# Performance work log

Hardware: AMD Instinct MI355X
Metric: run time of the kernel (lower is better)

The kernel has to match this reference:

```python
import jax, jax.numpy as jnp
import numpy as np
from jax import lax

B, D, H, W = 4, 32, 256, 256
ALPHA = 4.0     # init arg alpha
KFRAMES = 4.0   # self.K = alpha
EPS_BN = 1e-5

def FT2d(a):
    return jnp.fft.fft2(a, axes=(-2, -1))

def iFT2d(a):
    return jnp.fft.ifft2(a, axes=(-2, -1))

def forward_proj(field, otf):
    # field [B,D,H,W] real, otf [B,D,H,W] complex -> min-max scaled |holo| [B,1,H,W]
    Fholo = jnp.sum(FT2d(field.astype(jnp.complex64)) * otf, axis=1, keepdims=True)
    holo = jnp.abs(iFT2d(Fholo))
    mn = holo.min(axis=(-2, -1), keepdims=True)
    mx = holo.max(axis=(-2, -1), keepdims=True)
    return (holo - mn) / (mx - mn)

def back_proj(holo, otf):
    # holo [B,1,H,W] real -> real field [B,D,H,W]; broadcasting over depth == tile+FFT
    Fh = FT2d(holo.astype(jnp.complex64))
    return jnp.real(iFT2d(Fh * jnp.conj(otf)))

def cbl(xin, w, g, b, act):
    y = lax.conv_general_dilated(xin, w, (1, 1), 'SAME',
                                 dimension_numbers=('NCHW', 'OIHW', 'NCHW'))
    m = y.mean(axis=(0, 2, 3), keepdims=True)
    v = y.var(axis=(0, 2, 3), keepdims=True)  # biased var, torch BN training-mode
    y = (y - m) * lax.rsqrt(v + EPS_BN) * g[None, :, None, None] + b[None, :, None, None]
    return jax.nn.leaky_relu(y, 0.01) if act else y

def resblock(xin, wa, ga, ba, wb, gb, bb):
    h = cbl(cbl(xin, wa, ga, ba, True), wb, gb, bb, False)
    return jax.nn.leaky_relu(xin + h, 0.01)

def plholonet_forward(phi, z, u1, u2, otf, K1f, rho1, rho2, soft_thr, p):
    # ---- X update: FFT-domain proximal solve ----
    x1 = phi - u1
    x2 = z - u2
    n = rho1 * back_proj(x1, otf) + rho2 * x2
    d = (rho2 + jnp.abs(otf) ** 2 * rho1).astype(jnp.complex64)
    x = jnp.real(iFT2d(FT2d(n.astype(jnp.complex64)) / d))
    # ---- Phi update: vectorized 30-step masked bisection ----
    phi_tilde = forward_proj(x, otf) + u1
    K0 = 1.0 - K1f
    c = ALPHA / KFRAMES
    def func(y):
        return c * (K0 - K1f / (jnp.exp(c * y) - 1.0)) + rho1 * (y - phi_tilde)
    ind0_init = K1f == 0
    phimin = jnp.full_like(phi_tilde, 1e-5)
    phimax = jnp.full_like(phi_tilde, 100.0)
    phiave = 0.5 * (phimin + phimax)
    def step(carry, _):
        pmin, pmax, pave, ind0 = carry
        ind1 = jnp.logical_not(ind0)
        t = func(pave)
        pmin = jnp.where((t > 0) & ind1, pave, pmin)
        pmax = jnp.where((t < 0) & ind1, pave, pmax)
        ind0 = ind0 | ((t == 0) & ind1)
        pave = jnp.where(jnp.logical_not(ind0), 0.5 * (pmin + pmax), pave)
        return (pmin, pmax, pave, ind0), None
    (_, _, phiave, _), _ = lax.scan(step, (phimin, phimax, phiave, ind0_init), None, length=30)
    phi_next = jnp.where(ind0_init, phi_tilde - K0 / rho1, phiave)
    # ---- Z update: denoiser with symmetry loss ----
    z_tilde = x + u2
    h1 = resblock(z_tilde, p['w1a'], p['g1a'], p['b1a'], p['w1b'], p['g1b'], p['b1b'])
    h1_thr = jnp.sign(h1) * jax.nn.relu(jnp.abs(h1) - soft_thr)
    z_next = resblock(h1_thr, p['w2a'], p['g2a'], p['b2a'], p['w2b'], p['g2b'], p['b2b'])
    x_fb = resblock(h1, p['w2a'], p['g2a'], p['b2a'], p['w2b'], p['g2b'], p['b2b'])
    stage_symloss = x_fb - z_tilde
    # ---- dual updates ----
    u1_next = u1 + phi_next - forward_proj(x, otf)
    u2_next = u2 + z_next - x
    return (x, phi_next, z_next, u1_next, u2_next, stage_symloss)

def setup_inputs() -> dict:
    key = jax.random.key(0)
    ks = jax.random.split(key, 16)
    f = jnp.float32
    inp = dict(
        x=jax.random.normal(ks[0], (B, D, H, W), f),
        phi=jax.random.uniform(ks[1], (B, 1, H, W), dtype=f),
        z=jax.random.normal(ks[2], (B, D, H, W), f) * 0.1,
        u1=jax.random.uniform(ks[3], (B, 1, H, W), dtype=f) * 0.1,
        u2=jax.random.uniform(ks[4], (B, D, H, W), dtype=f) * 0.1,
        otf_real=jax.random.normal(ks[5], (B, D, H, W), f) * 0.5,
        otf_imag=jax.random.normal(ks[6], (B, D, H, W), f) * 0.5,
        K1=jax.random.randint(ks[7], (B, 1, H, W), 0, 5, jnp.int32),
        rho1=jnp.array([0.7], f),
        rho2=jnp.array([0.5], f),
        soft_thr=jnp.array([0.01], f),
    )
    for i, sfx in enumerate(['1a', '1b', '2a', '2b']):
        inp['w' + sfx] = jax.random.normal(ks[8 + i], (D, D, 3, 3), f) * 0.05
        inp['g' + sfx] = jnp.ones((D,), f)
        inp['b' + sfx] = jnp.zeros((D,), f)
    return inp

def reference(x, phi, z, u1, u2, otf_real, otf_imag, K1, rho1, rho2, soft_thr,
              w1a, g1a, b1a, w1b, g1b, b1b, w2a, g2a, b2a, w2b, g2b, b2b):
    # note: the torch forward immediately overwrites its `x` argument via X_update,
    # so the input x is unused (kept in the signature for interface faithfulness).
    otf = (otf_real + 1j * otf_imag).astype(jnp.complex64)
    K1f = K1.astype(jnp.float32)
    p = dict(w1a=w1a, g1a=g1a, b1a=b1a, w1b=w1b, g1b=g1b, b1b=b1b,
             w2a=w2a, g2a=g2a, b2a=b2a, w2b=w2b, g2b=g2b, b2b=b2b)
    return plholonet_forward(phi, z, u1, u2, otf, K1f, rho1, rho2, soft_thr, p)
```

## Files before the change

kernel.cpp:

```cpp
#include <hip/hip_runtime.h>
#include <math.h>

#define WDIM 256
#define HW   65536

struct cplx { float x, y; };
__device__ __forceinline__ cplx cmul(cplx a, cplx b){ return {a.x*b.x - a.y*b.y, a.x*b.y + a.y*b.x}; }
__device__ __forceinline__ cplx cadd(cplx a, cplx b){ return {a.x+b.x, a.y+b.y}; }
__device__ __forceinline__ cplx csub(cplx a, cplx b){ return {a.x-b.x, a.y-b.y}; }
__device__ __forceinline__ void swapc(cplx& a, cplx& b){ cplx t=a; a=b; b=t; }

typedef __attribute__((ext_vector_type(8))) short short8;
typedef __attribute__((ext_vector_type(4))) float float4v;

__device__ __forceinline__ unsigned short f2bf(float f){
  unsigned int u = __float_as_uint(f);
  unsigned int r = (u + 0x7FFFu + ((u >> 16) & 1u)) >> 16;
  return (unsigned short)r;
}
__device__ __forceinline__ float bf2f(unsigned short h){
  return __uint_as_float(((unsigned int)h) << 16);
}

template<bool INV>
__device__ __forceinline__ void fft16(cplx v[16]) {
  const float C16[8] = {1.f, 0.9238795325112867f, 0.7071067811865476f, 0.3826834323650898f,
                        0.f, -0.3826834323650898f, -0.7071067811865476f, -0.9238795325112867f};
  const float S16[8] = {0.f, 0.3826834323650898f, 0.7071067811865476f, 0.9238795325112867f,
                        1.f, 0.9238795325112867f, 0.7071067811865476f, 0.3826834323650898f};
  swapc(v[1], v[8]); swapc(v[2], v[4]); swapc(v[3], v[12]);
  swapc(v[5], v[10]); swapc(v[7], v[14]); swapc(v[11], v[13]);
  #pragma unroll
  for (int s = 1; s <= 4; ++s) {
    const int m = 1 << s, half = m >> 1, step = 16 >> s;
    #pragma unroll
    for (int k = 0; k < 16; k += m) {
      #pragma unroll
      for (int j = 0; j < half; ++j) {
        cplx w = {C16[j*step], INV ? S16[j*step] : -S16[j*step]};
        cplx t = cmul(w, v[k+j+half]);
        v[k+j+half] = csub(v[k+j], t);
        v[k+j]      = cadd(v[k+j], t);
      }
    }
  }
}

template<bool INV>
__device__ void fft256_16(cplx v[16], int t, cplx* Yu) {
  fft16<INV>(v);
  float ang = (INV ? 6.283185307179586f : -6.283185307179586f) * (float)t * (1.0f/256.0f);
  float sn, cs; sincosf(ang, &sn, &cs);
  cplx wstep = {cs, sn}, w = {1.f, 0.f};
  #pragma unroll
  for (int c = 0; c < 16; ++c) { v[c] = cmul(v[c], w); w = cmul(w, wstep); }
  __syncthreads();
  #pragma unroll
  for (int c = 0; c < 16; ++c) Yu[t*17 + c] = v[c];
  __syncthreads();
  cplx z[16];
  #pragma unroll
  for (int b = 0; b < 16; ++b) z[b] = Yu[b*17 + t];
  fft16<INV>(z);
  #pragma unroll
  for (int d = 0; d < 16; ++d) v[d] = z[d];
  __syncthreads();
}

__global__ __launch_bounds__(256) void k_row_fwd_all(const float* __restrict__ a,
                                                     const float* __restrict__ b,
                                                     const float* __restrict__ sa,
                                                     const float* __restrict__ sb,
                                                     cplx* __restrict__ P,
                                                     cplx* __restrict__ XS,
                                                     const float* __restrict__ w1a,
                                                     const float* __restrict__ w1b,
                                                     const float* __restrict__ w2a,
                                                     const float* __restrict__ w2b,
                                                     unsigned short* __restrict__ Ap) {
  __shared__ cplx Y[16*280];
  int bp = blockIdx.y;
  if (bp == 66) {
    int base = blockIdx.x * 2304;
    for (int r = threadIdx.x; r < 2304; r += 256) {
      int idx = base + r;
      int wsel = idx / 9216, rr = idx - wsel*9216;
      const float* w = wsel==0 ? w1a : wsel==1 ? w1b : wsel==2 ? w2a : w2b;
      int tap = rr / 1024, r2 = rr - tap*1024, oc = r2 >> 5, ic = r2 & 31;
      Ap[idx] = f2bf(w[(oc*32 + ic)*9 + tap]);
    }
    return;
  }
  int unit = threadIdx.x >> 4, t = threadIdx.x & 15;
  size_t rowoff = (size_t)(blockIdx.x*16 + unit)*WDIM;
  const float *pa, *pb;
  size_t base0, baseo_rel;
  cplx* outb;
  if (bp < 64) {
    int bb = bp >> 4, p = bp & 15;
    pa = a; pb = b;
    base0 = ((size_t)(bb*32 + 2*p))*HW + rowoff;
    outb = P; baseo_rel = (size_t)bp*HW + rowoff;
  } else {
    int pp = bp - 64;
    pa = sa; pb = sb;
    base0 = ((size_t)(2*pp))*HW + rowoff;
    outb = XS; baseo_rel = (size_t)pp*HW + rowoff;
  }
  size_t base1 = base0 + HW;
  cplx v[16];
  #pragma unroll
  for (int i = 0; i < 16; ++i) {
    size_t o = i*16 + t;
    v[i] = {pa[base0+o] - pb[base0+o], pa[base1+o] - pb[base1+o]};
  }
  fft256_16<false>(v, t, Y + unit*280);
  #pragma unroll
  for (int d = 0; d < 16; ++d) outb[baseo_rel + t + 16*d] = v[d];
}

template<bool INV>
__device__ void col_core(const cplx* __restrict__ in, cplx* lds, cplx v[16], size_t planeBase) {
  int tid = threadIdx.x;
  #pragma unroll
  for (int i = 0; i < 16; ++i) {
    int idx = tid + 256*i; int h = idx >> 4, w = idx & 15;
    lds[h*17 + w] = in[planeBase + (size_t)h*WDIM + w];
  }
  __syncthreads();
  int u = tid >> 4, t = tid & 15;
  cplx vv[16];
  #pragma unroll
  for (int a = 0; a < 16; ++a) vv[a] = lds[(16*a + t)*17 + u];
  fft256_16<INV>(vv, t, lds + u*280);
  #pragma unroll
  for (int d = 0; d < 16; ++d) v[d] = vv[d];
}

__global__ __launch_bounds__(256) void k_col_fwd_all(cplx* __restrict__ P,
                                                     cplx* __restrict__ XS) {
  __shared__ cplx lds[4480];
  int y = blockIdx.y;
  cplx* buf = (y < 64) ? (P + (size_t)y*HW) : (XS + (size_t)(y-64)*HW);
  size_t planeBase = blockIdx.x*16;
  cplx v[16];
  col_core<false>(buf, lds, v, planeBase);
  int u = threadIdx.x >> 4, t = threadIdx.x & 15;
  #pragma unroll
  for (int d = 0; d < 16; ++d) lds[(t + 16*d)*17 + u] = v[d];
  __syncthreads();
  int tid = threadIdx.x;
  #pragma unroll
  for (int i = 0; i < 16; ++i) {
    int idx = tid + 256*i; int h = idx >> 4, w = idx & 15;
    buf[planeBase + (size_t)h*WDIM + w] = lds[h*17 + w];
  }
}

__global__ __launch_bounds__(256) void k_combine_inv(const cplx* __restrict__ P,
                                                     const cplx* __restrict__ XS,
                                                     const float* __restrict__ otr,
                                                     const float* __restrict__ oti,
                                                     const float* __restrict__ r1p,
                                                     const float* __restrict__ r2p,
                                                     cplx* __restrict__ W2,
                                                     cplx* __restrict__ HFX) {
  __shared__ cplx R[16*273];
  int kw = threadIdx.x;
  int kh = blockIdx.x;
  int b  = blockIdx.y;
  int kh2 = (256 - kh) & 255;
  int kw2 = (256 - kw) & 255;
  int k  = (kh << 8) | kw;
  int k2 = (kh2 << 8) | kw2;
  float rho1 = r1p[0], rho2 = r2p[0];
  int c = b >> 1, par = b & 1;
  cplx Sk = XS[(c << 16) | k], Sm = XS[(c << 16) | k2];
  cplx A;
  if (par == 0) A = {0.5f*(Sk.x + Sm.x), 0.5f*(Sk.y - Sm.y)};
  else          A = {0.5f*(Sk.y + Sm.y), 0.5f*(Sm.x - Sk.x)};
  cplx Am = {A.x, -A.y};
  float hfr = 0.f, hfi = 0.f, hfr2 = 0.f, hfi2 = 0.f;
  int unit = threadIdx.x >> 4, t = threadIdx.x & 15;

  #pragma unroll 1
  for (int half = 0; half < 2; ++half) {
    #pragma unroll 1
    for (int pl = 0; pl < 8; ++pl) {
      int p = half*8 + pl;
      int pb = (b*16 + p) << 16;
      cplx Pk = P[pb | k], Pm = P[pb | k2];
      float Zr[2], Zi[2];
      Zr[0] = 0.5f*(Pk.x + Pm.x); Zi[0] = 0.5f*(Pk.y - Pm.y);
      Zr[1] = 0.5f*(Pk.y + Pm.y); Zi[1] = 0.5f*(Pm.x - Pk.x);
      float Xr[2], Xi[2];
      #pragma unroll
      for (int dd = 0; dd < 2; ++dd) {
        int db = (b*32 + 2*p + dd) << 16;
        float or1 = otr[db | k],  oi1 = oti[db | k];
        float or2 = otr[db | k2], oi2 = oti[db | k2];
        float Gr = 0.5f*(A.x*or1 + A.y*oi1 + Am.x*or2 + Am.y*oi2);
        float Gi = 0.5f*(A.y*or1 - A.x*oi1 + Am.x*oi2 - Am.y*or2);
        float di = 0.5f*(1.f/(rho2 + rho1*(or1*or1 + oi1*oi1))
                       + 1.f/(rho2 + rho1*(or2*or2 + oi2*oi2)));
        float xr = (rho1*Gr + rho2*Zr[dd])*di;
        float xi = (rho1*Gi + rho2*Zi[dd])*di;
        Xr[dd] = xr; Xi[dd] = xi;
        hfr  += xr*or1 - xi*oi1;
        hfi  += xr*oi1 + xi*or1;
        hfr2 += xr*or2 + xi*oi2;
        hfi2 += xr*oi2 - xi*or2;
      }
      R[(pl*2)*273 + kw]    = {Xr[0] - Xi[1], Xi[0] + Xr[1]};
      R[(pl*2+1)*273 + kw2] = {Xr[0] + Xi[1], Xr[1] - Xi[0]};
    }
    __syncthreads();
    {
      cplx* slot = R + unit*273;
      cplx v[16];
      #pragma unroll
      for (int i = 0; i < 16; ++i) v[i] = slot[i*16 + t];
      fft256_16<true>(v, t, slot);
      int plane = b*16 + half*8 + (unit >> 1);
      int row = (unit & 1) ? kh2 : kh;
      size_t base = (size_t)plane*HW + (size_t)row*WDIM;
      #pragma unroll
      for (int d = 0; d < 16; ++d)
        W2[base + t + 16*d] = {v[d].x*(1.f/256.f), v[d].y*(1.f/256.f)};
    }
  }
  R[0*273 + kw]  = {hfr,  hfi};
  R[1*273 + kw2] = {hfr2, hfi2};
  __syncthreads();
  {
    cplx* slot = R + (unit & 1)*273;
    cplx v[16];
    #pragma unroll
    for (int i = 0; i < 16; ++i) v[i] = slot[i*16 + t];
    fft256_16<true>(v, t, slot);
    if (unit < 2) {
      int row = unit ? kh2 : kh;
      size_t base = (size_t)b*HW + (size_t)row*WDIM;
      #pragma unroll
      for (int d = 0; d < 16; ++d)
        HFX[base + t + 16*d] = {v[d].x*(1.f/256.f), v[d].y*(1.f/256.f)};
    }
  }
}

__global__ __launch_bounds__(256) void k_col_inv_all(const cplx* __restrict__ W2,
                                                     const cplx* __restrict__ XS,
                                                     const float* __restrict__ u2,
                                                     float* __restrict__ xout,
                                                     unsigned short* __restrict__ ztcl,
                                                     float* __restrict__ holo,
                                                     float* __restrict__ partials) {
  __shared__ cplx lds[4480];
  int y = blockIdx.y;
  int tid = threadIdx.x;
  if (y < 64) {
    int bb = y >> 4, p = y & 15;
    cplx v[16];
    col_core<true>(W2 + (size_t)y*HW, lds, v, blockIdx.x*16);
    int u = tid >> 4, t = tid & 15;
    #pragma unroll
    for (int d = 0; d < 16; ++d) lds[(t + 16*d)*17 + u] = {v[d].x*(1.f/256.f), v[d].y*(1.f/256.f)};
    __syncthreads();
    size_t out0 = ((size_t)(bb*32 + 2*p))*HW + blockIdx.x*16;
    size_t out1 = out0 + HW;
    #pragma unroll
    for (int i = 0; i < 16; ++i) {
      int idx = tid + 256*i; int h = idx >> 4, w = idx & 15;
      cplx val = lds[h*17 + w];
      size_t g0 = out0 + (size_t)h*WDIM + w;
      size_t g1 = out1 + (size_t)h*WDIM + w;
      float zt0 = val.x + u2[g0];
      float zt1 = val.y + u2[g1];
      xout[g0] = val.x;
      xout[g1] = val.y;
      int pix = (h << 8) + (blockIdx.x << 4) + w;
      unsigned int pk = ((unsigned int)f2bf(zt1) << 16) | (unsigned int)f2bf(zt0);
      *(unsigned int*)(ztcl + ((((size_t)(bb << 16)) + pix) << 5) + 2*p) = pk;
    }
  } else {
    int py = y - 64;
    float* ldsf = (float*)lds;
    cplx v[16];
    col_core<true>(XS + (size_t)py*HW, lds, v, blockIdx.x*16);
    int u = tid >> 4, t = tid & 15;
    #pragma unroll
    for (int d = 0; d < 16; ++d) {
      float re = v[d].x*(1.f/256.f), im = v[d].y*(1.f/256.f);
      ldsf[(t + 16*d)*17 + u] = sqrtf(re*re + im*im);
    }
    __syncthreads();
    float mn = 1e30f, mx = -1e30f;
    size_t planeBase = (size_t)py*HW + blockIdx.x*16;
    #pragma unroll
    for (int i = 0; i < 16; ++i) {
      int idx = tid + 256*i; int h = idx >> 4, w = idx & 15;
      float val = ldsf[h*17 + w];
      holo[planeBase + (size_t)h*WDIM + w] = val;
      mn = fminf(mn, val); mx = fmaxf(mx, val);
    }
    __syncthreads();
    #pragma unroll
    for (int s = 1; s < 64; s <<= 1) { mn = fminf(mn, __shfl_xor(mn, s)); mx = fmaxf(mx, __shfl_xor(mx, s)); }
    if ((tid & 63) == 0) { ldsf[(tid>>6)*2] = mn; ldsf[(tid>>6)*2 + 1] = mx; }
    __syncthreads();
    if (tid == 0) {
      float a = fminf(fminf(ldsf[0], ldsf[2]), fminf(ldsf[4], ldsf[6]));
      float b = fmaxf(fmaxf(ldsf[1], ldsf[3]), fmaxf(ldsf[5], ldsf[7]));
      partials[(py*16 + blockIdx.x)*2]     = a;
      partials[(py*16 + blockIdx.x)*2 + 1] = b;
    }
  }
}

__global__ __launch_bounds__(256) void k_bisect(const float* __restrict__ holo,
                                                const float* __restrict__ partials,
                                                const float* __restrict__ u1,
                                                const int* __restrict__ K1,
                                                const float* __restrict__ r1p,
                                                float* __restrict__ phi_out,
                                                float* __restrict__ u1_out) {
  __shared__ float red2[2];
  int i = blockIdx.x*256 + threadIdx.x;
  int b = i >> 16;
  if (threadIdx.x < 16) {
    float mn = partials[(b*16 + threadIdx.x)*2];
    float mx = partials[(b*16 + threadIdx.x)*2 + 1];
    #pragma unroll
    for (int s = 1; s < 16; s <<= 1) { mn = fminf(mn, __shfl_xor(mn, s)); mx = fmaxf(mx, __shfl_xor(mx, s)); }
    if (threadIdx.x == 0) { red2[0] = mn; red2[1] = mx; }
  }
  __syncthreads();
  float mn = red2[0], mx = red2[1];
  float fp = (holo[i] - mn) / (mx - mn);
  float pt = fp + u1[i];
  float K1f = (float)K1[i];
  float K0 = 1.f - K1f;
  float rho1 = r1p[0];
  bool ind0i = (K1f == 0.f);
  bool ind0 = ind0i;
  float pmin = 1e-5f, pmax = 100.f, pave = 0.5f*(pmin + pmax);
  #pragma unroll 1
  for (int it = 0; it < 30; ++it) {
    float e = expf(pave);
    float t = (K0 - K1f/(e - 1.f)) + rho1*(pave - pt);
    bool ind1 = !ind0;
    if (t > 0.f && ind1) pmin = pave;
    if (t < 0.f && ind1) pmax = pave;
    ind0 = ind0 || (t == 0.f && ind1);
    if (!ind0) pave = 0.5f*(pmin + pmax);
  }
  float pn = ind0i ? (pt - K0/rho1) : pave;
  phi_out[i] = pn;
  u1_out[i]  = u1[i] + pn - fp;
}

#define CONV_R 4
__global__ __launch_bounds__(256, 4) void k_conv(const unsigned short* __restrict__ inCL,
                                                 const unsigned short* __restrict__ Aprep,
                                                 unsigned short* __restrict__ outCL,
                                                 float* __restrict__ part,
                                                 int mode,
                                                 const float* __restrict__ scsh,
                                                 const float* __restrict__ thrp) {
  __shared__ unsigned short tile[6*66*32];
  __shared__ float sred[4][16][2];
  int tid = threadIdx.x;
  int bx = blockIdx.x, by = blockIdx.y, bz = blockIdx.z;
  int w0 = bx*64, h0 = by*CONV_R;

  for (int idx = tid; idx < 6*264; idx += 256) {
    int lrow = idx/264, rem = idx - lrow*264;
    int lcol = rem >> 2, m = rem & 3;
    int grow = h0 - 1 + lrow, gcol = w0 - 1 + lcol;
    uint4 val = {0,0,0,0};
    if (grow >= 0 && grow < 256 && gcol >= 0 && gcol < 256) {
      uint4 raw = *(const uint4*)(inCL + (((size_t)(bz<<16) + (grow<<8) + gcol)<<5) + m*8);
      if (mode == 0) val = raw;
      else {
        unsigned short h8[8]; *(uint4*)h8 = raw;
        #pragma unroll
        for (int j = 0; j < 8; ++j) {
          float v = bf2f(h8[j]);
          int ic = m*8+j; v = v*scsh[ic] + scsh[32+ic]; v = v > 0.f ? v : 0.01f*v;
          h8[j] = f2bf(v);
        }
        val = *(uint4*)h8;
      }
    }
    *(uint4*)&tile[(size_t)idx*8] = val;
  }

  int lane = tid & 63, w = tid >> 6;
  int q = lane >> 4, ln = lane & 15;
  int ocH = w & 1, s0 = w >> 1;
  short8 afrag[9];
  #pragma unroll
  for (int t = 0; t < 9; ++t)
    afrag[t] = *(const short8*)(Aprep + ((t*32 + ocH*16 + ln)*32 + q*8));
  __syncthreads();

  float sacc[4] = {0,0,0,0}, s2acc[4] = {0,0,0,0};
  #pragma unroll
  for (int r = 0; r < CONV_R; ++r) {
    #pragma unroll
    for (int si = 0; si < 2; ++si) {
      int s = s0 + si*2;
      float4v acc = {0.f, 0.f, 0.f, 0.f};
      #pragma unroll
      for (int t = 0; t < 9; ++t) {
        int dy = t/3, dx = t - dy*3;
        int lrow = r + dy, lcol = s*16 + ln + dx;
        const short8 bfrag = *(const short8*)&tile[(lrow*66 + lcol)*32 + q*8];
        acc = __builtin_amdgcn_mfma_f32_16x16x32_bf16(afrag[t], bfrag, acc, 0, 0, 0);
      }
      int px = w0 + s*16 + ln, row = h0 + r;
      size_t obase = ((((size_t)(bz<<16) + (row<<8) + px))<<5) + ocH*16 + q*4;
      unsigned short o4[4];
      #pragma unroll
      for (int u = 0; u < 4; ++u) { o4[u] = f2bf(acc[u]); sacc[u] += acc[u]; s2acc[u] += acc[u]*acc[u]; }
      *(uint2*)(outCL + obase) = *(uint2*)o4;
    }
  }

  #pragma unroll
  for (int u = 0; u < 4; ++u) {
    float a = sacc[u], b2 = s2acc[u];
    #pragma unroll
    for (int mq = 1; mq < 16; mq <<= 1) { a += __shfl_xor(a, mq); b2 += __shfl_xor(b2, mq); }
    if (ln == 0) { sred[w][q*4+u][0] = a; sred[w][q*4+u][1] = b2; }
  }
  __syncthreads();
  if (tid < 64) {
    int ocH2 = tid >> 5, i16 = (tid >> 1) & 15, st = tid & 1;
    float tot = sred[ocH2][i16][st] + sred[ocH2+2][i16][st];
    int oc = ocH2*16 + i16;
    int blk = ((bz<<6) + by)*4 + bx;
    part[(oc*2+st)*1024 + blk] = tot;
  }
}

__global__ __launch_bounds__(256, 3) void k_conv35(const unsigned short* __restrict__ ztcl,
                                                   const unsigned short* __restrict__ c2,
                                                   const unsigned short* __restrict__ Aprep,
                                                   unsigned short* __restrict__ outT,
                                                   unsigned short* __restrict__ outR,
                                                   float* __restrict__ partT,
                                                   float* __restrict__ partR,
                                                   const float* __restrict__ ss1,
                                                   const float* __restrict__ thrp) {
  __shared__ unsigned short tileR[6*66*32];
  __shared__ unsigned short tileT[6*66*32];
  __shared__ float sredT[4][16][2];
  __shared__ float sredR[4][16][2];
  int tid = threadIdx.x;
  int bx = blockIdx.x, by = blockIdx.y, bz = blockIdx.z;
  int w0 = bx*64, h0 = by*CONV_R;
  float thr = thrp[0];

  for (int idx = tid; idx < 6*264; idx += 256) {
    int lrow = idx/264, rem = idx - lrow*264;
    int lcol = rem >> 2, m = rem & 3;
    int grow = h0 - 1 + lrow, gcol = w0 - 1 + lcol;
    uint4 rawv = {0,0,0,0}, thrv = {0,0,0,0};
    if (grow >= 0 && grow < 256 && gcol >= 0 && gcol < 256) {
      size_t gaddr = (((size_t)(bz<<16) + (grow<<8) + gcol)<<5) + m*8;
      uint4 az = *(const uint4*)(ztcl + gaddr);
      uint4 ac = *(const uint4*)(c2 + gaddr);
      unsigned short z8[8], cc8[8], h8[8], t8[8];
      *(uint4*)z8 = az; *(uint4*)cc8 = ac;
      #pragma unroll
      for (int j = 0; j < 8; ++j) {
        int ic = m*8 + j;
        float v = bf2f(z8[j]) + bf2f(cc8[j])*ss1[ic] + ss1[32+ic];
        v = v > 0.f ? v : 0.01f*v;
        h8[j] = f2bf(v);
        float hb = bf2f(h8[j]);
        float s = fabsf(hb) - thr; s = s > 0.f ? s : 0.f;
        t8[j] = f2bf(copysignf(s, hb));
      }
      rawv = *(uint4*)h8;
      thrv = *(uint4*)t8;
    }
    *(uint4*)&tileR[(size_t)idx*8] = rawv;
    *(uint4*)&tileT[(size_t)idx*8] = thrv;
  }

  int lane = tid & 63, w = tid >> 6;
  int q = lane >> 4, ln = lane & 15;
  int ocH = w & 1, s0 = w >> 1;
  short8 afrag[9];
  #pragma unroll
  for (int t = 0; t < 9; ++t)
    afrag[t] = *(const short8*)(Aprep + ((t*32 + ocH*16 + ln)*32 + q*8));
  __syncthreads();

  float saT[4] = {0,0,0,0}, s2T[4] = {0,0,0,0};
  float saR[4] = {0,0,0,0}, s2R[4] = {0,0,0,0};
  #pragma unroll
  for (int r = 0; r < CONV_R; ++r) {
    #pragma unroll
    for (int si = 0; si < 2; ++si) {
      int s = s0 + si*2;
      float4v accT = {0.f,0.f,0.f,0.f}, accR = {0.f,0.f,0.f,0.f};
      #pragma unroll
      for (int t = 0; t < 9; ++t) {
        int dy = t/3, dx = t - dy*3;
        int lrow = r + dy, lcol = s*16 + ln + dx;
        size_t off = ((size_t)(lrow*66 + lcol))*32 + q*8;
        const short8 bT = *(const short8*)&tileT[off];
        accT = __builtin_amdgcn_mfma_f32_16x16x32_bf16(afrag[t], bT, accT, 0, 0, 0);
        const short8 bR = *(const short8*)&tileR[off];
        accR = __builtin_amdgcn_mfma_f32_16x16x32_bf16(afrag[t], bR, accR, 0, 0, 0);
      }
      int px = w0 + s*16 + ln, row = h0 + r;
      size_t obase = ((((size_t)(bz<<16) + (row<<8) + px))<<5) + ocH*16 + q*4;
      unsigned short oT[4], oR[4];
      #pragma unroll
      for (int u = 0; u < 4; ++u) {
        oT[u] = f2bf(accT[u]); saT[u] += accT[u]; s2T[u] += accT[u]*accT[u];
        oR[u] = f2bf(accR[u]); saR[u] += accR[u]; s2R[u] += accR[u]*accR[u];
      }
      *(uint2*)(outT + obase) = *(uint2*)oT;
      *(uint2*)(outR + obase) = *(uint2*)oR;
    }
  }

  #pragma unroll
  for (int u = 0; u < 4; ++u) {
    float aT = saT[u], bT2 = s2T[u], aR = saR[u], bR2 = s2R[u];
    #pragma unroll
    for (int mq = 1; mq < 16; mq <<= 1) {
      aT += __shfl_xor(aT, mq); bT2 += __shfl_xor(bT2, mq);
      aR += __shfl_xor(aR, mq); bR2 += __shfl_xor(bR2, mq);
    }
    if (ln == 0) {
      sredT[w][q*4+u][0] = aT; sredT[w][q*4+u][1] = bT2;
      sredR[w][q*4+u][0] = aR; sredR[w][q*4+u][1] = bR2;
    }
  }
  __syncthreads();
  if (tid < 64) {
    int ocH2 = tid >> 5, i16 = (tid >> 1) & 15, st = tid & 1;
    int oc = ocH2*16 + i16;
    int blk = ((bz<<6) + by)*4 + bx;
    partT[(oc*2+st)*1024 + blk] = sredT[ocH2][i16][st] + sredT[ocH2+2][i16][st];
    partR[(oc*2+st)*1024 + blk] = sredR[ocH2][i16][st] + sredR[ocH2+2][i16][st];
  }
}

__global__ __launch_bounds__(256, 4) void k_conv_pair(const unsigned short* __restrict__ inA,
                                                      const unsigned short* __restrict__ inB,
                                                      unsigned short* __restrict__ outA,
                                                      unsigned short* __restrict__ outB,
                                                      float* __restrict__ partA,
                                                      float* __restrict__ partB,
                                                      const float* __restrict__ ssA,
                                                      const float* __restrict__ ssB,
                                                      const unsigned short* __restrict__ Aprep) {
  __shared__ unsigned short tile[6*66*32];
  __shared__ float sred[4][16][2];
  int tid = threadIdx.x;
  int bx = blockIdx.x, by = blockIdx.y;
  int half = blockIdx.z >> 2, bz = blockIdx.z & 3;
  const unsigned short* inCL = half ? inB : inA;
  unsigned short* outCL = half ? outB : outA;
  const float* scsh = half ? ssB : ssA;
  float* part = half ? partB : partA;
  int w0 = bx*64, h0 = by*CONV_R;

  for (int idx = tid; idx < 6*264; idx += 256) {
    int lrow = idx/264, rem = idx - lrow*264;
    int lcol = rem >> 2, m = rem & 3;
    int grow = h0 - 1 + lrow, gcol = w0 - 1 + lcol;
    uint4 val = {0,0,0,0};
    if (grow >= 0 && grow < 256 && gcol >= 0 && gcol < 256) {
      uint4 raw = *(const uint4*)(inCL + (((size_t)(bz<<16) + (grow<<8) + gcol)<<5) + m*8);
      unsigned short h8[8]; *(uint4*)h8 = raw;
      #pragma unroll
      for (int j = 0; j < 8; ++j) {
        float v = bf2f(h8[j]);
        int ic = m*8+j; v = v*scsh[ic] + scsh[32+ic]; v = v > 0.f ? v : 0.01f*v;
        h8[j] = f2bf(v);
      }
      val = *(uint4*)h8;
    }
    *(uint4*)&tile[(size_t)idx*8] = val;
  }

  int lane = tid & 63, w = tid >> 6;
  int q = lane >> 4, ln = lane & 15;
  int ocH = w & 1, s0 = w >> 1;
  short8 afrag[9];
  #pragma unroll
  for (int t = 0; t < 9; ++t)
    afrag[t] = *(const short8*)(Aprep + ((t*32 + ocH*16 + ln)*32 + q*8));
  __syncthreads();

  float sacc[4] = {0,0,0,0}, s2acc[4] = {0,0,0,0};
  #pragma unroll
  for (int r = 0; r < CONV_R; ++r) {
    #pragma unroll
    for (int si = 0; si < 2; ++si) {
      int s = s0 + si*2;
      float4v acc = {0.f, 0.f, 0.f, 0.f};
      #pragma unroll
      for (int t = 0; t < 9; ++t) {
        int dy = t/3, dx = t - dy*3;
        int lrow = r + dy, lcol = s*16 + ln + dx;
        const short8 bfrag = *(const short8*)&tile[(lrow*66 + lcol)*32 + q*8];
        acc = __builtin_amdgcn_mfma_f32_16x16x32_bf16(afrag[t], bfrag, acc, 0, 0, 0);
      }
      int px = w0 + s*16 + ln, row = h0 + r;
      size_t obase = ((((size_t)(bz<<16) + (row<<8) + px))<<5) + ocH*16 + q*4;
      unsigned short o4[4];
      #pragma unroll
      for (int u = 0; u < 4; ++u) { o4[u] = f2bf(acc[u]); sacc[u] += acc[u]; s2acc[u] += acc[u]*acc[u]; }
      *(uint2*)(outCL + obase) = *(uint2*)o4;
    }
  }

  #pragma unroll
  for (int u = 0; u < 4; ++u) {
    float a = sacc[u], b2 = s2acc[u];
    #pragma unroll
    for (int mq = 1; mq < 16; mq <<= 1) { a += __shfl_xor(a, mq); b2 += __shfl_xor(b2, mq); }
    if (ln == 0) { sred[w][q*4+u][0] = a; sred[w][q*4+u][1] = b2; }
  }
  __syncthreads();
  if (tid < 64) {
    int ocH2 = tid >> 5, i16 = (tid >> 1) & 15, st = tid & 1;
    float tot = sred[ocH2][i16][st] + sred[ocH2+2][i16][st];
    int oc = ocH2*16 + i16;
    int blk = ((bz<<6) + by)*4 + bx;
    part[(oc*2+st)*1024 + blk] = tot;
  }
}

__global__ __launch_bounds__(256) void k_finstats2(const float* __restrict__ part,
                                                   const float* __restrict__ g,
                                                   const float* __restrict__ beta,
                                                   float* __restrict__ SS) {
  __shared__ float red[8];
  int oc = blockIdx.x, t = threadIdx.x;
  const float* ps = part + oc*2048;
  float s  = ps[t] + ps[t+256] + ps[t+512] + ps[t+768];
  float s2 = ps[1024+t] + ps[1280+t] + ps[1536+t] + ps[1792+t];
  #pragma unroll
  for (int m = 1; m < 64; m <<= 1) { s += __shfl_xor(s, m); s2 += __shfl_xor(s2, m); }
  if ((t & 63) == 0) { red[(t>>6)*2] = s; red[(t>>6)*2+1] = s2; }
  __syncthreads();
  if (t == 0) {
    float S  = red[0] + red[2] + red[4] + red[6];
    float S2 = red[1] + red[3] + red[5] + red[7];
    const float N = 262144.f;
    float mean = S / N;
    float var  = S2 / N - mean*mean;
    float sc = g[oc] * rsqrtf(var + 1e-5f);
    SS[oc] = sc; SS[32+oc] = beta[oc] - mean*sc;
  }
}

__global__ __launch_bounds__(256) void k_finstats_dual(const float* __restrict__ pA,
                                                       const float* __restrict__ pB,
                                                       const float* __restrict__ g,
                                                       const float* __restrict__ beta,
                                                       float* __restrict__ SSa,
                                                       float* __restrict__ SSc) {
  __shared__ float red[8];
  int bxi = blockIdx.x;
  const float* part = bxi < 32 ? pA : pB;
  float* SS = bxi < 32 ? SSa : SSc;
  int oc = bxi & 31, t = threadIdx.x;
  const float* ps = part + oc*2048;
  float s  = ps[t] + ps[t+256] + ps[t+512] + ps[t+768];
  float s2 = ps[1024+t] + ps[1280+t] + ps[1536+t] + ps[1792+t];
  #pragma unroll
  for (int m = 1; m < 64; m <<= 1) { s += __shfl_xor(s, m); s2 += __shfl_xor(s2, m); }
  if ((t & 63) == 0) { red[(t>>6)*2] = s; red[(t>>6)*2+1] = s2; }
  __syncthreads();
  if (t == 0) {
    float S  = red[0] + red[2] + red[4] + red[6];
    float S2 = red[1] + red[3] + red[5] + red[7];
    const float N = 262144.f;
    float mean = S / N;
    float var  = S2 / N - mean*mean;
    float sc = g[oc] * rsqrtf(var + 1e-5f);
    SS[oc] = sc; SS[32+oc] = beta[oc] - mean*sc;
  }
}

__global__ __launch_bounds__(256) void k_finalAB(const unsigned short* __restrict__ ztcl,
                                                 const unsigned short* __restrict__ c2,
                                                 const unsigned short* __restrict__ c4,
                                                 const unsigned short* __restrict__ c6,
                                                 const float* __restrict__ SS1,
                                                 const float* __restrict__ SS4,
                                                 const float* __restrict__ SS6,
                                                 const float* __restrict__ thrp,
                                                 const float* __restrict__ x,
                                                 float* __restrict__ zout,
                                                 float* __restrict__ u2out,
                                                 float* __restrict__ symout) {
  __shared__ float zT[32*66];
  __shared__ float uT[32*66];
  __shared__ float sT[32*66];
  int tid = threadIdx.x;
  size_t b = blockIdx.y;
  int px0 = blockIdx.x*64;
  float thr = thrp[0];
  int px = tid >> 2, cg = tid & 3;
  size_t cbase = ((((b<<16) + px0 + px))<<5) + cg*8;
  uint4 za  = *(const uint4*)(ztcl + cbase);
  uint4 c2a = *(const uint4*)(c2 + cbase);
  uint4 c4a = *(const uint4*)(c4 + cbase);
  uint4 c6a = *(const uint4*)(c6 + cbase);
  unsigned short zs[8], c2s[8], c4s[8], c6s[8];
  *(uint4*)zs = za; *(uint4*)c2s = c2a; *(uint4*)c4s = c4a; *(uint4*)c6s = c6a;
  #pragma unroll
  for (int j = 0; j < 8; ++j) {
    int c = cg*8+j;
    float ztv = bf2f(zs[j]);
    float h0 = ztv + bf2f(c2s[j])*SS1[c] + SS1[32+c];
    h0 = h0 > 0.f ? h0 : 0.01f*h0;
    float hv = bf2f(f2bf(h0));
    float s = fabsf(hv) - thr; s = s > 0.f ? s : 0.f;
    float th = copysignf(s, hv);
    float zv = th + bf2f(c4s[j])*SS4[c] + SS4[32+c];
    zv = zv > 0.f ? zv : 0.01f*zv;
    float xv = hv + bf2f(c6s[j])*SS6[c] + SS6[32+c];
    xv = xv > 0.f ? xv : 0.01f*xv;
    zT[c*66 + px] = zv;
    uT[c*66 + px] = zv + ztv;
    sT[c*66 + px] = xv - ztv;
  }
  __syncthreads();
  #pragma unroll
  for (int i = 0; i < 2; ++i) {
    int ch = tid + i*256; int c = ch >> 4, p4 = (ch & 15)*4;
    size_t g = ((b*32 + c)<<16) + px0 + p4;
    float4 xv = *(const float4*)(x + g);
    float4 zv = { zT[c*66+p4], zT[c*66+p4+1], zT[c*66+p4+2], zT[c*66+p4+3] };
    float4 un = { uT[c*66+p4]   - 2.f*xv.x, uT[c*66+p4+1] - 2.f*xv.y,
                  uT[c*66+p4+2] - 2.f*xv.z, uT[c*66+p4+3] - 2.f*xv.w };
    float4 sv = { sT[c*66+p4], sT[c*66+p4+1], sT[c*66+p4+2], sT[c*66+p4+3] };
    *(float4*)(zout + g) = zv;
    *(float4*)(u2out + g) = un;
    *(float4*)(symout + g) = sv;
  }
}

extern "C" void kernel_launch(void* const* d_in, const int* in_sizes, int n_in,
                              void* d_out, int out_size, void* d_ws, size_t ws_size,
                              hipStream_t stream) {
  const float* phi  = (const float*)d_in[1];
  const float* z    = (const float*)d_in[2];
  const float* u1   = (const float*)d_in[3];
  const float* u2   = (const float*)d_in[4];
  const float* otr  = (const float*)d_in[5];
  const float* oti  = (const float*)d_in[6];
  const int*   K1   = (const int*)d_in[7];
  const float* rho1 = (const float*)d_in[8];
  const float* rho2 = (const float*)d_in[9];
  const float* sthr = (const float*)d_in[10];
  const float* w1a = (const float*)d_in[11];
  const float* g1a = (const float*)d_in[12];
  const float* b1a = (const float*)d_in[13];
  const float* w1b = (const float*)d_in[14];
  const float* g1b = (const float*)d_in[15];
  const float* b1b = (const float*)d_in[16];
  const float* w2a = (const float*)d_in[17];
  const float* g2a = (const float*)d_in[18];
  const float* b2a = (const float*)d_in[19];
  const float* w2b = (const float*)d_in[20];
  const float* g2b = (const float*)d_in[21];
  const float* b2b = (const float*)d_in[22];

  float* out = (float*)d_out;
  float* x_out   = out;
  float* phi_out = out + 8388608;
  float* z_out   = out + 8650752;
  float* u1_out  = out + 17039360;
  float* u2_out  = out + 17301504;
  float* sym_out = out + 25690112;

  char* ws = (char*)d_ws;
  cplx*  P     = (cplx*)ws;
  cplx*  XS    = (cplx*)(ws + 67108864);
  cplx*  HFX   = (cplx*)(ws + 69206016);
  float* holo  = (float*)(ws + 71303168);
  float* partmm= (float*)(ws + 72351744);

  unsigned short* Ap    = (unsigned short*)(ws + 68157440);
  float*          part  = (float*)(ws + 71434240);
  float*          partB = (float*)(ws + 69206016);
  float*          SSb   = (float*)(ws + 71696384);
  unsigned short* ZTcl  = (unsigned short*)(ws + 33554432);
  unsigned short* C2cl  = (unsigned short*)(ws + 16777216);
  unsigned short* C4cl  = (unsigned short*)(ws + 0);
  unsigned short* C6cl  = (unsigned short*)(ws + 50331648);
  unsigned short* C135a = (unsigned short*)z_out;
  unsigned short* C135b = (unsigned short*)((char*)z_out + 16777216);
  cplx* W2 = (cplx*)z_out;

  k_row_fwd_all <<<dim3(16, 67), 256, 0, stream>>>(z, u2, phi, u1, P, XS,
                                                   w1a, w1b, w2a, w2b, Ap);
  k_col_fwd_all <<<dim3(16, 66), 256, 0, stream>>>(P, XS);
  k_combine_inv <<<dim3(129, 4), 256, 0, stream>>>(P, XS, otr, oti, rho1, rho2, W2, HFX);
  k_col_inv_all <<<dim3(16, 68), 256, 0, stream>>>(W2, HFX, u2, x_out, ZTcl, holo, partmm);
  k_bisect<<<1024, 256, 0, stream>>>(holo, partmm, u1, K1, rho1, phi_out, u1_out);

  dim3 cg(4, 64, 4);
  k_conv<<<cg, 256, 0, stream>>>(ZTcl, Ap + 0,      C135a, part, 0, SSb,     sthr);
  k_finstats2<<<32, 256, 0, stream>>>(part, g1a, b1a, SSb + 0);
  k_conv<<<cg, 256, 0, stream>>>(C135a, Ap + 9216,  C2cl,  part, 1, SSb + 0, sthr);
  k_finstats2<<<32, 256, 0, stream>>>(part, g1b, b1b, SSb + 64);

  k_conv35<<<cg, 256, 0, stream>>>(ZTcl, C2cl, Ap + 18432, C135a, C135b,
                                   part, partB, SSb + 64, sthr);
  k_finstats_dual<<<64, 256, 0, stream>>>(part, partB, g2a, b2a, SSb + 128, SSb + 256);
  k_conv_pair<<<dim3(4, 64, 8), 256, 0, stream>>>(C135a, C135b, C4cl, C6cl,
                                                  part, partB, SSb + 128, SSb + 256,
                                                  Ap + 27648);
  k_finstats_dual<<<64, 256, 0, stream>>>(part, partB, g2b, b2b, SSb + 192, SSb + 320);

  k_finalAB<<<dim3(1024, 4), 256, 0, stream>>>(ZTcl, C2cl, C4cl, C6cl,
                                               SSb + 64, SSb + 192, SSb + 320, sthr,
                                               x_out, z_out, u2_out, sym_out);
}
```

Before: 469.0 us.

## Reorder forward 2D FFT: column pass first, fuse row pass into combine kernel

The forward FFT now does the column transform directly from the raw inputs in the first kernel. The row transform moves into the combine kernel, which loads the needed rows (kh and its mirror kh2) into LDS and transforms them before the Hermitian combine. This removes the separate column-FFT kernel and one full read-write pass of the 64 MB complex intermediate. In exchange the combine kernel does redundant row FFTs for mirror rows, needs more LDS, and adds synchronisation.

```diff
diff --git a/kernel.cpp b/kernel.cpp
--- a/kernel.cpp
+++ b/kernel.cpp
@@ -67,18 +67,18 @@
   __syncthreads();
 }
 
-__global__ __launch_bounds__(256) void k_row_fwd_all(const float* __restrict__ a,
-                                                     const float* __restrict__ b,
-                                                     const float* __restrict__ sa,
-                                                     const float* __restrict__ sb,
-                                                     cplx* __restrict__ P,
-                                                     cplx* __restrict__ XS,
-                                                     const float* __restrict__ w1a,
-                                                     const float* __restrict__ w1b,
-                                                     const float* __restrict__ w2a,
-                                                     const float* __restrict__ w2b,
-                                                     unsigned short* __restrict__ Ap) {
-  __shared__ cplx Y[16*280];
+__global__ __launch_bounds__(256) void k_fwd1(const float* __restrict__ a,
+                                              const float* __restrict__ b,
+                                              const float* __restrict__ sa,
+                                              const float* __restrict__ sb,
+                                              cplx* __restrict__ Pc,
+                                              cplx* __restrict__ XSc,
+                                              const float* __restrict__ w1a,
+                                              const float* __restrict__ w1b,
+                                              const float* __restrict__ w2a,
+                                              const float* __restrict__ w2b,
+                                              unsigned short* __restrict__ Ap) {
+  __shared__ cplx lds[4480];
   int bp = blockIdx.y;
   if (bp == 66) {
     int base = blockIdx.x * 2304;
@@ -91,81 +91,55 @@
     }
     return;
   }
-  int unit = threadIdx.x >> 4, t = threadIdx.x & 15;
-  size_t rowoff = (size_t)(blockIdx.x*16 + unit)*WDIM;
+  int tid = threadIdx.x;
   const float *pa, *pb;
-  size_t base0, baseo_rel;
+  size_t base0, baseo;
   cplx* outb;
   if (bp < 64) {
     int bb = bp >> 4, p = bp & 15;
     pa = a; pb = b;
-    base0 = ((size_t)(bb*32 + 2*p))*HW + rowoff;
-    outb = P; baseo_rel = (size_t)bp*HW + rowoff;
+    base0 = ((size_t)(bb*32 + 2*p))*HW;
+    outb = Pc; baseo = (size_t)bp*HW;
   } else {
     int pp = bp - 64;
     pa = sa; pb = sb;
-    base0 = ((size_t)(2*pp))*HW + rowoff;
-    outb = XS; baseo_rel = (size_t)pp*HW + rowoff;
+    base0 = ((size_t)(2*pp))*HW;
+    outb = XSc; baseo = (size_t)pp*HW;
   }
   size_t base1 = base0 + HW;
-  cplx v[16];
-  #pragma unroll
-  for (int i = 0; i < 16; ++i) {
-    size_t o = i*16 + t;
-    v[i] = {pa[base0+o] - pb[base0+o], pa[base1+o] - pb[base1+o]};
-  }
-  fft256_16<false>(v, t, Y + unit*280);
-  #pragma unroll
-  for (int d = 0; d < 16; ++d) outb[baseo_rel + t + 16*d] = v[d];
-}
-
-template<bool INV>
-__device__ void col_core(const cplx* __restrict__ in, cplx* lds, cplx v[16], size_t planeBase) {
-  int tid = threadIdx.x;
+  int w0 = blockIdx.x*16;
   #pragma unroll
   for (int i = 0; i < 16; ++i) {
     int idx = tid + 256*i; int h = idx >> 4, w = idx & 15;
-    lds[h*17 + w] = in[planeBase + (size_t)h*WDIM + w];
+    size_t g0 = base0 + (size_t)h*WDIM + w0 + w;
+    size_t g1 = base1 + (size_t)h*WDIM + w0 + w;
+    lds[h*17 + w] = {pa[g0] - pb[g0], pa[g1] - pb[g1]};
   }
   __syncthreads();
   int u = tid >> 4, t = tid & 15;
   cplx vv[16];
   #pragma unroll
-  for (int a = 0; a < 16; ++a) vv[a] = lds[(16*a + t)*17 + u];
-  fft256_16<INV>(vv, t, lds + u*280);
-  #pragma unroll
-  for (int d = 0; d < 16; ++d) v[d] = vv[d];
-}
-
-__global__ __launch_bounds__(256) void k_col_fwd_all(cplx* __restrict__ P,
-                                                     cplx* __restrict__ XS) {
-  __shared__ cplx lds[4480];
-  int y = blockIdx.y;
-  cplx* buf = (y < 64) ? (P + (size_t)y*HW) : (XS + (size_t)(y-64)*HW);
-  size_t planeBase = blockIdx.x*16;
-  cplx v[16];
-  col_core<false>(buf, lds, v, planeBase);
-  int u = threadIdx.x >> 4, t = threadIdx.x & 15;
-  #pragma unroll
-  for (int d = 0; d < 16; ++d) lds[(t + 16*d)*17 + u] = v[d];
-  __syncthreads();
-  int tid = threadIdx.x;
+  for (int a2 = 0; a2 < 16; ++a2) vv[a2] = lds[(16*a2 + t)*17 + u];
+  fft256_16<false>(vv, t, lds + u*280);
+  #pragma unroll
+  for (int d = 0; d < 16; ++d) lds[(t + 16*d)*17 + u] = vv[d];
+  __syncthreads();
   #pragma unroll
   for (int i = 0; i < 16; ++i) {
     int idx = tid + 256*i; int h = idx >> 4, w = idx & 15;
-    buf[planeBase + (size_t)h*WDIM + w] = lds[h*17 + w];
-  }
-}
-
-__global__ __launch_bounds__(256) void k_combine_inv(const cplx* __restrict__ P,
-                                                     const cplx* __restrict__ XS,
+    outb[baseo + (size_t)h*WDIM + w0 + w] = lds[h*17 + w];
+  }
+}
+
+__global__ __launch_bounds__(256) void k_combine_inv(const cplx* __restrict__ Pc,
+                                                     const cplx* __restrict__ XSc,
                                                      const float* __restrict__ otr,
                                                      const float* __restrict__ oti,
                                                      const float* __restrict__ r1p,
                                                      const float* __restrict__ r2p,
                                                      cplx* __restrict__ W2,
                                                      cplx* __restrict__ HFX) {
-  __shared__ cplx R[16*273];
+  __shared__ cplx R[18*273];
   int kw = threadIdx.x;
   int kh = blockIdx.x;
   int b  = blockIdx.y;
@@ -175,21 +149,53 @@
   int k2 = (kh2 << 8) | kw2;
   float rho1 = r1p[0], rho2 = r2p[0];
   int c = b >> 1, par = b & 1;
-  cplx Sk = XS[(c << 16) | k], Sm = XS[(c << 16) | k2];
+  int unit = kw >> 4, t = kw & 15;
+
+  R[16*273 + kw] = XSc[(size_t)c*HW + (size_t)kh*WDIM + kw];
+  R[17*273 + kw] = XSc[(size_t)c*HW + (size_t)kh2*WDIM + kw];
+  __syncthreads();
+  {
+    cplx v[16];
+    cplx* slot = R + (16 + (unit & 1))*273;
+    #pragma unroll
+    for (int i = 0; i < 16; ++i) v[i] = slot[i*16 + t];
+    fft256_16<false>(v, t, slot);
+    #pragma unroll
+    for (int d = 0; d < 16; ++d) slot[t + 16*d] = v[d];
+  }
+  __syncthreads();
+  cplx Sk = R[16*273 + kw], Sm = R[17*273 + kw2];
   cplx A;
   if (par == 0) A = {0.5f*(Sk.x + Sm.x), 0.5f*(Sk.y - Sm.y)};
   else          A = {0.5f*(Sk.y + Sm.y), 0.5f*(Sm.x - Sk.x)};
   cplx Am = {A.x, -A.y};
   float hfr = 0.f, hfi = 0.f, hfr2 = 0.f, hfi2 = 0.f;
-  int unit = threadIdx.x >> 4, t = threadIdx.x & 15;
 
   #pragma unroll 1
   for (int half = 0; half < 2; ++half) {
     #pragma unroll 1
+    for (int idx = kw; idx < 16*256; idx += 256) {
+      int sl = idx >> 8, w = idx & 255;
+      int p = half*8 + (sl >> 1);
+      int row = (sl & 1) ? kh2 : kh;
+      R[sl*273 + w] = Pc[(size_t)(b*16 + p)*HW + (size_t)row*WDIM + w];
+    }
+    __syncthreads();
+    {
+      cplx v[16];
+      cplx* slot = R + unit*273;
+      #pragma unroll
+      for (int i = 0; i < 16; ++i) v[i] = slot[i*16 + t];
+      fft256_16<false>(v, t, slot);
+      #pragma unroll
+      for (int d = 0; d < 16; ++d) slot[t + 16*d] = v[d];
+    }
+    __syncthreads();
+    #pragma unroll 1
     for (int pl = 0; pl < 8; ++pl) {
       int p = half*8 + pl;
-      int pb = (b*16 + p) << 16;
-      cplx Pk = P[pb | k], Pm = P[pb | k2];
+      cplx Pk = R[(pl*2)*273 + kw];
+      cplx Pm = R[(pl*2+1)*273 + kw2];
       float Zr[2], Zi[2];
       Zr[0] = 0.5f*(Pk.x + Pm.x); Zi[0] = 0.5f*(Pk.y - Pm.y);
       Zr[1] = 0.5f*(Pk.y + Pm.y); Zi[1] = 0.5f*(Pm.x - Pk.x);
@@ -216,8 +222,8 @@
     }
     __syncthreads();
     {
+      cplx v[16];
       cplx* slot = R + unit*273;
-      cplx v[16];
       #pragma unroll
       for (int i = 0; i < 16; ++i) v[i] = slot[i*16 + t];
       fft256_16<true>(v, t, slot);
@@ -246,6 +252,24 @@
         HFX[base + t + 16*d] = {v[d].x*(1.f/256.f), v[d].y*(1.f/256.f)};
     }
   }
+}
+
+template<bool INV>
+__device__ void col_core(const cplx* __restrict__ in, cplx* lds, cplx v[16], size_t planeBase) {
+  int tid = threadIdx.x;
+  #pragma unroll
+  for (int i = 0; i < 16; ++i) {
+    int idx = tid + 256*i; int h = idx >> 4, w = idx & 15;
+    lds[h*17 + w] = in[planeBase + (size_t)h*WDIM + w];
+  }
+  __syncthreads();
+  int u = tid >> 4, t = tid & 15;
+  cplx vv[16];
+  #pragma unroll
+  for (int a = 0; a < 16; ++a) vv[a] = lds[(16*a + t)*17 + u];
+  fft256_16<INV>(vv, t, lds + u*280);
+  #pragma unroll
+  for (int d = 0; d < 16; ++d) v[d] = vv[d];
 }
 
 __global__ __launch_bounds__(256) void k_col_inv_all(const cplx* __restrict__ W2,
@@ -789,8 +813,8 @@
   float* sym_out = out + 25690112;
 
   char* ws = (char*)d_ws;
-  cplx*  P     = (cplx*)ws;
-  cplx*  XS    = (cplx*)(ws + 67108864);
+  cplx*  Pc    = (cplx*)ws;
+  cplx*  XSc   = (cplx*)(ws + 67108864);
   cplx*  HFX   = (cplx*)(ws + 69206016);
   float* holo  = (float*)(ws + 71303168);
   float* partmm= (float*)(ws + 72351744);
@@ -807,10 +831,9 @@
   unsigned short* C135b = (unsigned short*)((char*)z_out + 16777216);
   cplx* W2 = (cplx*)z_out;
 
-  k_row_fwd_all <<<dim3(16, 67), 256, 0, stream>>>(z, u2, phi, u1, P, XS,
+  k_fwd1        <<<dim3(16, 67), 256, 0, stream>>>(z, u2, phi, u1, Pc, XSc,
                                                    w1a, w1b, w2a, w2b, Ap);
-  k_col_fwd_all <<<dim3(16, 66), 256, 0, stream>>>(P, XS);
-  k_combine_inv <<<dim3(129, 4), 256, 0, stream>>>(P, XS, otr, oti, rho1, rho2, W2, HFX);
+  k_combine_inv <<<dim3(129, 4), 256, 0, stream>>>(Pc, XSc, otr, oti, rho1, rho2, W2, HFX);
   k_col_inv_all <<<dim3(16, 68), 256, 0, stream>>>(W2, HFX, u2, x_out, ZTcl, holo, partmm);
   k_bisect<<<1024, 256, 0, stream>>>(holo, partmm, u1, K1, rho1, phi_out, u1_out);
 
```

Measured after the change: 500.8 us. +6.8%, slower.

## Split combine kernel over plane halves and finish hologram FFT separately

Applied to the files above, without the earlier changes.

The combine/inverse-row kernel now runs two plane-groups as separate blocks (grid z=2) instead of looping over both halves serially, doubling the block count from 516 to 1032. Each group writes its partial hologram spectrum sums to its own buffer. A new small kernel adds the two partials and performs the row inverse FFT for HFX. This exposes more parallelism in a kernel that was under-occupied, at the cost of an extra launch, extra global traffic for the partial buffers, and new workspace aliasing.

```diff
diff --git a/kernel.cpp b/kernel.cpp
--- a/kernel.cpp
+++ b/kernel.cpp
@@ -157,18 +157,20 @@
   }
 }
 
-__global__ __launch_bounds__(256) void k_combine_inv(const cplx* __restrict__ P,
-                                                     const cplx* __restrict__ XS,
-                                                     const float* __restrict__ otr,
-                                                     const float* __restrict__ oti,
-                                                     const float* __restrict__ r1p,
-                                                     const float* __restrict__ r2p,
-                                                     cplx* __restrict__ W2,
-                                                     cplx* __restrict__ HFX) {
+__global__ __launch_bounds__(256) void k_combine_half(const cplx* __restrict__ P,
+                                                      const cplx* __restrict__ XS,
+                                                      const float* __restrict__ otr,
+                                                      const float* __restrict__ oti,
+                                                      const float* __restrict__ r1p,
+                                                      const float* __restrict__ r2p,
+                                                      cplx* __restrict__ W2,
+                                                      cplx* __restrict__ HFa,
+                                                      cplx* __restrict__ HFb) {
   __shared__ cplx R[16*273];
   int kw = threadIdx.x;
   int kh = blockIdx.x;
   int b  = blockIdx.y;
+  int g  = blockIdx.z;
   int kh2 = (256 - kh) & 255;
   int kw2 = (256 - kw) & 255;
   int k  = (kh << 8) | kw;
@@ -181,71 +183,72 @@
   else          A = {0.5f*(Sk.y + Sm.y), 0.5f*(Sm.x - Sk.x)};
   cplx Am = {A.x, -A.y};
   float hfr = 0.f, hfi = 0.f, hfr2 = 0.f, hfi2 = 0.f;
-  int unit = threadIdx.x >> 4, t = threadIdx.x & 15;
+  int unit = kw >> 4, t = kw & 15;
 
   #pragma unroll 1
-  for (int half = 0; half < 2; ++half) {
-    #pragma unroll 1
-    for (int pl = 0; pl < 8; ++pl) {
-      int p = half*8 + pl;
-      int pb = (b*16 + p) << 16;
-      cplx Pk = P[pb | k], Pm = P[pb | k2];
-      float Zr[2], Zi[2];
-      Zr[0] = 0.5f*(Pk.x + Pm.x); Zi[0] = 0.5f*(Pk.y - Pm.y);
-      Zr[1] = 0.5f*(Pk.y + Pm.y); Zi[1] = 0.5f*(Pm.x - Pk.x);
-      float Xr[2], Xi[2];
-      #pragma unroll
-      for (int dd = 0; dd < 2; ++dd) {
-        int db = (b*32 + 2*p + dd) << 16;
-        float or1 = otr[db | k],  oi1 = oti[db | k];
-        float or2 = otr[db | k2], oi2 = oti[db | k2];
-        float Gr = 0.5f*(A.x*or1 + A.y*oi1 + Am.x*or2 + Am.y*oi2);
-        float Gi = 0.5f*(A.y*or1 - A.x*oi1 + Am.x*oi2 - Am.y*or2);
-        float di = 0.5f*(1.f/(rho2 + rho1*(or1*or1 + oi1*oi1))
-                       + 1.f/(rho2 + rho1*(or2*or2 + oi2*oi2)));
-        float xr = (rho1*Gr + rho2*Zr[dd])*di;
-        float xi = (rho1*Gi + rho2*Zi[dd])*di;
-        Xr[dd] = xr; Xi[dd] = xi;
-        hfr  += xr*or1 - xi*oi1;
-        hfi  += xr*oi1 + xi*or1;
-        hfr2 += xr*or2 + xi*oi2;
-        hfi2 += xr*oi2 - xi*or2;
-      }
-      R[(pl*2)*273 + kw]    = {Xr[0] - Xi[1], Xi[0] + Xr[1]};
-      R[(pl*2+1)*273 + kw2] = {Xr[0] + Xi[1], Xr[1] - Xi[0]};
-    }
-    __syncthreads();
-    {
-      cplx* slot = R + unit*273;
-      cplx v[16];
-      #pragma unroll
-      for (int i = 0; i < 16; ++i) v[i] = slot[i*16 + t];
-      fft256_16<true>(v, t, slot);
-      int plane = b*16 + half*8 + (unit >> 1);
-      int row = (unit & 1) ? kh2 : kh;
-      size_t base = (size_t)plane*HW + (size_t)row*WDIM;
-      #pragma unroll
-      for (int d = 0; d < 16; ++d)
-        W2[base + t + 16*d] = {v[d].x*(1.f/256.f), v[d].y*(1.f/256.f)};
-    }
-  }
-  R[0*273 + kw]  = {hfr,  hfi};
-  R[1*273 + kw2] = {hfr2, hfi2};
+  for (int pl = 0; pl < 8; ++pl) {
+    int p = g*8 + pl;
+    int pb = (b*16 + p) << 16;
+    cplx Pk = P[pb | k], Pm = P[pb | k2];
+    float Zr[2], Zi[2];
+    Zr[0] = 0.5f*(Pk.x + Pm.x); Zi[0] = 0.5f*(Pk.y - Pm.y);
+    Zr[1] = 0.5f*(Pk.y + Pm.y); Zi[1] = 0.5f*(Pm.x - Pk.x);
+    float Xr[2], Xi[2];
+    #pragma unroll
+    for (int dd = 0; dd < 2; ++dd) {
+      int db = (b*32 + 2*p + dd) << 16;
+      float or1 = otr[db | k],  oi1 = oti[db | k];
+      float or2 = otr[db | k2], oi2 = oti[db | k2];
+      float Gr = 0.5f*(A.x*or1 + A.y*oi1 + Am.x*or2 + Am.y*oi2);
+      float Gi = 0.5f*(A.y*or1 - A.x*oi1 + Am.x*oi2 - Am.y*or2);
+      float di = 0.5f*(1.f/(rho2 + rho1*(or1*or1 + oi1*oi1))
+                     + 1.f/(rho2 + rho1*(or2*or2 + oi2*oi2)));
+      float xr = (rho1*Gr + rho2*Zr[dd])*di;
+      float xi = (rho1*Gi + rho2*Zi[dd])*di;
+      Xr[dd] = xr; Xi[dd] = xi;
+      hfr  += xr*or1 - xi*oi1;
+      hfi  += xr*oi1 + xi*or1;
+      hfr2 += xr*or2 + xi*oi2;
+      hfi2 += xr*oi2 - xi*or2;
+    }
+    R[(pl*2)*273 + kw]    = {Xr[0] - Xi[1], Xi[0] + Xr[1]};
+    R[(pl*2+1)*273 + kw2] = {Xr[0] + Xi[1], Xr[1] - Xi[0]};
+  }
   __syncthreads();
   {
-    cplx* slot = R + (unit & 1)*273;
+    cplx* slot = R + unit*273;
     cplx v[16];
     #pragma unroll
     for (int i = 0; i < 16; ++i) v[i] = slot[i*16 + t];
     fft256_16<true>(v, t, slot);
-    if (unit < 2) {
-      int row = unit ? kh2 : kh;
-      size_t base = (size_t)b*HW + (size_t)row*WDIM;
-      #pragma unroll
-      for (int d = 0; d < 16; ++d)
-        HFX[base + t + 16*d] = {v[d].x*(1.f/256.f), v[d].y*(1.f/256.f)};
-    }
-  }
+    int plane = b*16 + g*8 + (unit >> 1);
+    int row = (unit & 1) ? kh2 : kh;
+    size_t base = (size_t)plane*HW + (size_t)row*WDIM;
+    #pragma unroll
+    for (int d = 0; d < 16; ++d)
+      W2[base + t + 16*d] = {v[d].x*(1.f/256.f), v[d].y*(1.f/256.f)};
+  }
+  cplx* HFo = g ? HFb : HFa;
+  HFo[(b << 16) | k]  = {hfr,  hfi};
+  HFo[(b << 16) | k2] = {hfr2, hfi2};
+}
+
+__global__ __launch_bounds__(256) void k_hf_fin(const cplx* __restrict__ Ha,
+                                                const cplx* __restrict__ Hb,
+                                                cplx* __restrict__ HFX) {
+  __shared__ cplx Y[16*280];
+  int unit = threadIdx.x >> 4, t = threadIdx.x & 15;
+  size_t base = (size_t)blockIdx.y*HW + (size_t)(blockIdx.x*16 + unit)*WDIM;
+  cplx v[16];
+  #pragma unroll
+  for (int i = 0; i < 16; ++i) {
+    cplx a = Ha[base + i*16 + t], bb = Hb[base + i*16 + t];
+    v[i] = {a.x + bb.x, a.y + bb.y};
+  }
+  fft256_16<true>(v, t, Y + unit*280);
+  #pragma unroll
+  for (int d = 0; d < 16; ++d)
+    HFX[base + t + 16*d] = {v[d].x*(1.f/256.f), v[d].y*(1.f/256.f)};
 }
 
 __global__ __launch_bounds__(256) void k_col_inv_all(const cplx* __restrict__ W2,
@@ -791,11 +794,13 @@
   char* ws = (char*)d_ws;
   cplx*  P     = (cplx*)ws;
   cplx*  XS    = (cplx*)(ws + 67108864);
-  cplx*  HFX   = (cplx*)(ws + 69206016);
   float* holo  = (float*)(ws + 71303168);
   float* partmm= (float*)(ws + 72351744);
 
   unsigned short* Ap    = (unsigned short*)(ws + 68157440);
+  cplx*  HFa   = (cplx*)(ws + 69206016);
+  cplx*  HFb   = (cplx*)(ws + 50331648);
+  cplx*  HFX   = (cplx*)(ws + 52428800);
   float*          part  = (float*)(ws + 71434240);
   float*          partB = (float*)(ws + 69206016);
   float*          SSb   = (float*)(ws + 71696384);
@@ -810,7 +815,9 @@
   k_row_fwd_all <<<dim3(16, 67), 256, 0, stream>>>(z, u2, phi, u1, P, XS,
                                                    w1a, w1b, w2a, w2b, Ap);
   k_col_fwd_all <<<dim3(16, 66), 256, 0, stream>>>(P, XS);
-  k_combine_inv <<<dim3(129, 4), 256, 0, stream>>>(P, XS, otr, oti, rho1, rho2, W2, HFX);
+  k_combine_half<<<dim3(129, 4, 2), 256, 0, stream>>>(P, XS, otr, oti, rho1, rho2,
+                                                      W2, HFa, HFb);
+  k_hf_fin      <<<dim3(16, 4), 256, 0, stream>>>(HFa, HFb, HFX);
   k_col_inv_all <<<dim3(16, 68), 256, 0, stream>>>(W2, HFX, u2, x_out, ZTcl, holo, partmm);
   k_bisect<<<1024, 256, 0, stream>>>(holo, partmm, u1, K1, rho1, phi_out, u1_out);
 
```

New measurement: 477.8 us. About the same (+1.9%).
